# Kernel tuning notes

Measured on AMD Instinct MI355X. Metric: run time of the kernel, lower is better.

The kernel has to match this reference:

```python
import jax, jax.numpy as jnp
import numpy as np

B, M, N, D, H = 4, 8, 128, 32, 64
SMALL_V = 1e-8


def setup_inputs() -> dict:
    key = jax.random.key(0)
    ks = jax.random.split(key, 12)
    s = 0.05
    x = jax.random.normal(ks[0], (B, M, N, D), jnp.float32)
    sizes = jax.random.randint(ks[1], (B,), N // 2, N + 1)
    valid = (jnp.arange(N)[None, :] < sizes[:, None]).astype(jnp.float32)  # [B,N]
    x = x * valid[:, None, :, None]  # zero out padded items
    return {
        "x": x,
        "x_size": sizes.astype(jnp.float32),
        "W1a": jax.random.normal(ks[2], (D, 2 * D), jnp.float32) * s,
        "b1a": jax.random.normal(ks[3], (2 * D,), jnp.float32) * s,
        "W1b": jax.random.normal(ks[4], (2 * D, D), jnp.float32) * s,
        "b1b": jax.random.normal(ks[5], (D,), jnp.float32) * s,
        "W2a": jax.random.normal(ks[6], (D, 2 * D), jnp.float32) * s,
        "b2a": jax.random.normal(ks[7], (2 * D,), jnp.float32) * s,
        "W2b": jax.random.normal(ks[8], (2 * D, H), jnp.float32) * s,
        "b2b": jax.random.normal(ks[9], (H,), jnp.float32) * s,
        "w3": jax.random.normal(ks[10], (H,), jnp.float32) * s,
        "b3": jax.random.normal(ks[11], (1,), jnp.float32) * s,
    }


def _item_mask(x):
    # 1.0 where the item's feature row has any nonzero entry, else 0.0. [...,N,1]
    return jnp.any(x != 0, axis=-1, keepdims=True).astype(x.dtype)


def _set_norm(x, x_size):
    # layer_normalization with is_set_norm=True: normalize over (N*D) per set,
    # dividing by the true valid size x_size*D and masking padded items.
    b, m, n, d = x.shape
    mask = jnp.broadcast_to(_item_mask(x), x.shape).reshape(b, m, n * d)
    xr = x.reshape(b, m, n * d)
    denom = x_size[:, None] * d  # [B,1] -> broadcasts over nSet
    mean = jnp.sum(xr, axis=-1) / denom  # [B,M]
    diff = xr - mean[..., None]
    std = jnp.sqrt(jnp.sum(diff * diff * mask, axis=-1) / denom)  # [B,M]
    out = diff / (std[..., None] + SMALL_V) * mask
    return out.reshape(b, m, n, d)


def reference(x, x_size, W1a, b1a, W1b, b1b, W2a, b2a, W2b, b2b, w3, b3):
    mask = _item_mask(x)  # [B,M,N,1]
    x_orig = x
    xn = _set_norm(x, x_size) * mask  # [B,M,N,D]
    # MLP1 (rank-4 -> masked by its own input's item mask)
    m1 = _item_mask(xn)
    x1 = (jnp.matmul(jax.nn.gelu(jnp.matmul(xn, W1a) + b1a), W1b) + b1b) * m1
    # pairwise differences: x_diff[b,m,i,j,:] = x1[b,m,i,:] - xn[b,m,j,:]
    x_diff = x1[:, :, :, None, :] - xn[:, :, None, :, :]  # [B,M,N,N,D]
    # MLP2 (rank-5 -> no mask, is_SoftMax=0)
    e = jnp.matmul(jax.nn.gelu(jnp.matmul(x_diff, W2a) + b2a), W2b) + b2b  # [B,M,N,N,H]
    # aggregation: out[b,m,j,h,d] = sum_i e[b,m,i,j,h] * x1[b,m,i,d]
    agg = jnp.einsum('bmijh,bmid->bmjhd', e, x1)
    # MLP3_linear: Dense(1) over H, then squeeze
    out = jnp.einsum('bmjhd,h->bmjd', agg, w3) + b3[0]
    out = (out + x_orig) * mask
    return out
```

## Files before the change

kernel.cpp:

```cpp
#include <hip/hip_runtime.h>

#define NNC 128
#define DDC 32
#define KKC 64
constexpr int ND = NNC * DDC;
#define SMALLV 1e-8f

__device__ __forceinline__ float gelu_f(float v) {
    float v2 = v * v;
    float p  = fmaf(0.1029432f, v2, 2.3022082f);
    float e  = __builtin_amdgcn_exp2f(v * p);
    float r  = __builtin_amdgcn_rcpf(e + 1.0f);
    return fmaf(-v, r, v);
}

__global__ __launch_bounds__(512, 1) void fused3(
    const float* __restrict__ x, const float* __restrict__ x_size,
    const float* __restrict__ W1a, const float* __restrict__ b1a,
    const float* __restrict__ W1b, const float* __restrict__ b1b,
    const float* __restrict__ W2a, const float* __restrict__ b2a,
    const float* __restrict__ W2b, const float* __restrict__ b2b,
    const float* __restrict__ w3, const float* __restrict__ b3,
    float* __restrict__ out)
{
    __shared__ __align__(16) float smem[16384];

    const int t   = threadIdx.x;
    const int blk = blockIdx.x;
    const int bm  = blk >> 3;
    const int jt  = blk & 7;
    const int k   = t & 63;
    const int w   = t >> 6;
    const int dL  = t & 31;

    const int iN = (int)(x_size[bm >> 3] + 0.5f);

    float* sX1  = smem;
    float* sA1  = smem + 4096;
    float* sXn  = smem + 4096;
    float* sH32 = smem + 8192;
    float* scr  = smem + 12800;
    float* sA2t = smem + 12800;
    float* sSt  = smem + 13888;
    float* sV2  = smem + 16000;
    float* sAny = smem + 16064;
    float* sRed = smem + 16192;
    float* sC3  = smem + 16200;

    if (jt * 16 >= iN) {
        out[(size_t)bm * ND + jt * 512 + t] = 0.f;
        return;
    }

    float colA[32];
    #pragma unroll
    for (int d = 0; d < 32; ++d) colA[d] = W1a[d * 64 + k];
    float colB[64];
    #pragma unroll
    for (int q = 0; q < 64; ++q) colB[q] = W1b[q * 32 + dL];
    const float rb1a = b1a[k];
    const float rb1b = b1b[dL];
    const float rb2a = b2a[k];

    {
        const int kk = t >> 3, hq = t & 7;
        float p = 0.f;
        #pragma unroll
        for (int h = 0; h < 8; ++h)
            p = fmaf(W2b[kk * 64 + hq * 8 + h], w3[hq * 8 + h], p);
        scr[t] = p;
    }
    if (t < 64) {
        float q = b2b[t] * w3[t];
        #pragma unroll
        for (int off = 32; off; off >>= 1) q += __shfl_xor(q, off);
        if (t == 0) sC3[0] = q;
    }
    if (t < 128) sAny[t] = 0.f;
    __syncthreads();

    const float4* xs4 = (const float4*)(x + (size_t)bm * ND);
    float4 v4[2];
    float lsum = 0.f;
    #pragma unroll
    for (int s = 0; s < 2; ++s) {
        int f = t + s * 512;
        float4 q = xs4[f];
        v4[s] = q;
        lsum += q.x + q.y + q.z + q.w;
        if (q.x != 0.f || q.y != 0.f || q.z != 0.f || q.w != 0.f) sAny[f >> 3] = 1.f;
    }
    #pragma unroll
    for (int off = 32; off; off >>= 1) lsum += __shfl_xor(lsum, off);
    if ((t & 63) == 0) sRed[w] = lsum;
    __syncthreads();
    if (t < 64) {
        float vp = 0.f;
        #pragma unroll
        for (int q = 0; q < 8; ++q) vp += scr[t * 8 + q];
        sV2[t] = vp;
    }
    const float denom = x_size[bm >> 3] * 32.f;
    float mean = 0.f;
    #pragma unroll
    for (int r = 0; r < 8; ++r) mean += sRed[r];
    mean /= denom;

    float lsq = 0.f;
    #pragma unroll
    for (int s = 0; s < 2; ++s) {
        int f = t + s * 512;
        float mk = sAny[f >> 3];
        float dx = v4[s].x - mean, dy = v4[s].y - mean;
        float dz = v4[s].z - mean, dw = v4[s].w - mean;
        lsq += mk * (dx * dx + dy * dy + dz * dz + dw * dw);
    }
    #pragma unroll
    for (int off = 32; off; off >>= 1) lsq += __shfl_xor(lsq, off);
    __syncthreads();
    if ((t & 63) == 0) sRed[w] = lsq;
    __syncthreads();
    float sq = 0.f;
    #pragma unroll
    for (int r = 0; r < 8; ++r) sq += sRed[r];
    const float inv = 1.f / (sqrtf(sq / denom) + SMALLV);

    #pragma unroll
    for (int s = 0; s < 2; ++s) {
        int f = t + s * 512;
        float mk = sAny[f >> 3] * inv;
        float4 q = v4[s];
        q.x = (q.x - mean) * mk; q.y = (q.y - mean) * mk;
        q.z = (q.z - mean) * mk; q.w = (q.w - mean) * mk;
        ((float4*)sXn)[f] = q;
    }
    __syncthreads();

    for (int c = 0; c < 4; ++c) {
        const int rb = c * 32;
        const bool live = (rb < iN);
        if (live) {
            #pragma unroll
            for (int r = 0; r < 4; ++r) {
                const int nl = w + 8 * r;
                const float4* xr4 = (const float4*)&sXn[(rb + nl) * 32];
                float acc = rb1a;
                #pragma unroll
                for (int dq = 0; dq < 8; ++dq) {
                    float4 xv = xr4[dq];
                    acc = fmaf(xv.x, colA[4 * dq + 0], acc);
                    acc = fmaf(xv.y, colA[4 * dq + 1], acc);
                    acc = fmaf(xv.z, colA[4 * dq + 2], acc);
                    acc = fmaf(xv.w, colA[4 * dq + 3], acc);
                }
                sH32[nl * 64 + k] = gelu_f(acc);
            }
        }
        __syncthreads();
        if (live) {
            #pragma unroll
            for (int p = 0; p < 2; ++p) {
                const int nl = (t >> 5) + 16 * p;
                const float4* hr4 = (const float4*)&sH32[nl * 64];
                float acc = rb1b;
                #pragma unroll
                for (int qq = 0; qq < 16; ++qq) {
                    float4 hv = hr4[qq];
                    acc = fmaf(hv.x, colB[4 * qq + 0], acc);
                    acc = fmaf(hv.y, colB[4 * qq + 1], acc);
                    acc = fmaf(hv.z, colB[4 * qq + 2], acc);
                    acc = fmaf(hv.w, colB[4 * qq + 3], acc);
                }
                sX1[(rb + nl) * 32 + dL] = acc * sAny[rb + nl];
            }
        } else {
            #pragma unroll
            for (int p = 0; p < 2; ++p)
                sX1[(rb + (t >> 5) + 16 * p) * 32 + dL] = 0.f;
        }
        __syncthreads();
    }

    float colC[32];
    #pragma unroll
    for (int d = 0; d < 32; ++d) colC[d] = W2a[d * 64 + k];
    #pragma unroll
    for (int q = 0; q < 2; ++q) {
        const int jl = w + 8 * q;
        const float4* xr4 = (const float4*)&sXn[(jt * 16 + jl) * 32];
        float acc = 0.f;
        #pragma unroll
        for (int dq = 0; dq < 8; ++dq) {
            float4 xv = xr4[dq];
            acc = fmaf(xv.x, colC[4 * dq + 0], acc);
            acc = fmaf(xv.y, colC[4 * dq + 1], acc);
            acc = fmaf(xv.z, colC[4 * dq + 2], acc);
            acc = fmaf(xv.w, colC[4 * dq + 3], acc);
        }
        sA2t[jl * 68 + k] = acc;
    }
    __syncthreads();

    const int ICAP = (iN + 3) & ~3;
    for (int n = w; n < ICAP; n += 8) {
        const float4* x14 = (const float4*)&sX1[n * 32];
        float acc = rb2a;
        #pragma unroll
        for (int dq = 0; dq < 8; ++dq) {
            float4 xv = x14[dq];
            acc = fmaf(xv.x, colC[4 * dq + 0], acc);
            acc = fmaf(xv.y, colC[4 * dq + 1], acc);
            acc = fmaf(xv.z, colC[4 * dq + 2], acc);
            acc = fmaf(xv.w, colC[4 * dq + 3], acc);
        }
        sA1[n * 68 + k] = acc;
    }
    __syncthreads();

    {
        const float c3 = sC3[0];
        const int j  = t & 15;
        const int i0 = (t >> 4) * 4;
        if (i0 < iN) {
            float a0 = c3, a1 = c3, a2 = c3, a3 = c3;
            const float* a2row = &sA2t[j * 68];
            const float* b0r = &sA1[(i0 + 0) * 68];
            const float* b1r = &sA1[(i0 + 1) * 68];
            const float* b2r = &sA1[(i0 + 2) * 68];
            const float* b3r = &sA1[(i0 + 3) * 68];
            #pragma unroll 4
            for (int kk = 0; kk < 64; kk += 4) {
                float4 va = *(const float4*)&a2row[kk];
                float4 vv = *(const float4*)&sV2[kk];
                float4 q0 = *(const float4*)&b0r[kk];
                float4 q1 = *(const float4*)&b1r[kk];
                float4 q2 = *(const float4*)&b2r[kk];
                float4 q3 = *(const float4*)&b3r[kk];
                a0 = fmaf(gelu_f(q0.x - va.x), vv.x, a0);
                a1 = fmaf(gelu_f(q1.x - va.x), vv.x, a1);
                a2 = fmaf(gelu_f(q2.x - va.x), vv.x, a2);
                a3 = fmaf(gelu_f(q3.x - va.x), vv.x, a3);
                a0 = fmaf(gelu_f(q0.y - va.y), vv.y, a0);
                a1 = fmaf(gelu_f(q1.y - va.y), vv.y, a1);
                a2 = fmaf(gelu_f(q2.y - va.y), vv.y, a2);
                a3 = fmaf(gelu_f(q3.y - va.y), vv.y, a3);
                a0 = fmaf(gelu_f(q0.z - va.z), vv.z, a0);
                a1 = fmaf(gelu_f(q1.z - va.z), vv.z, a1);
                a2 = fmaf(gelu_f(q2.z - va.z), vv.z, a2);
                a3 = fmaf(gelu_f(q3.z - va.z), vv.z, a3);
                a0 = fmaf(gelu_f(q0.w - va.w), vv.w, a0);
                a1 = fmaf(gelu_f(q1.w - va.w), vv.w, a1);
                a2 = fmaf(gelu_f(q2.w - va.w), vv.w, a2);
                a3 = fmaf(gelu_f(q3.w - va.w), vv.w, a3);
            }
            *(float4*)&sSt[j * 132 + i0] = make_float4(a0, a1, a2, a3);
        }
    }
    __syncthreads();

    {
        const int jA = t >> 5;
        const int dA = t & 31;
        const float* strow = &sSt[jA * 132];
        float s0 = 0.f;
        for (int i = 0; i < ICAP; i += 4) {
            float4 sv = *(const float4*)&strow[i];
            s0 = fmaf(sv.x, sX1[(i + 0) * 32 + dA], s0);
            s0 = fmaf(sv.y, sX1[(i + 1) * 32 + dA], s0);
            s0 = fmaf(sv.z, sX1[(i + 2) * 32 + dA], s0);
            s0 = fmaf(sv.w, sX1[(i + 3) * 32 + dA], s0);
        }
        const int jg = jt * 16 + jA;
        const float msk = sAny[jg];
        const size_t ob = (size_t)bm * ND + jg * 32 + dA;
        out[ob] = (s0 + b3[0] + x[ob]) * msk;
    }
}

extern "C" void kernel_launch(void* const* d_in, const int* in_sizes, int n_in,
                              void* d_out, int out_size, void* d_ws, size_t ws_size,
                              hipStream_t stream) {
    (void)in_sizes; (void)n_in; (void)d_ws; (void)ws_size; (void)out_size;
    const float* x      = (const float*)d_in[0];
    const float* x_size = (const float*)d_in[1];
    const float* W1a    = (const float*)d_in[2];
    const float* b1a    = (const float*)d_in[3];
    const float* W1b    = (const float*)d_in[4];
    const float* b1b    = (const float*)d_in[5];
    const float* W2a    = (const float*)d_in[6];
    const float* b2a    = (const float*)d_in[7];
    const float* W2b    = (const float*)d_in[8];
    const float* b2b    = (const float*)d_in[9];
    const float* w3     = (const float*)d_in[10];
    const float* b3     = (const float*)d_in[11];
    float* out = (float*)d_out;

    fused3<<<dim3(256), dim3(512), 0, stream>>>(
        x, x_size, W1a, b1a, W1b, b1b, W2a, b2a, W2b, b2b, w3, b3, out);
}
```

Measured before the change: 99.42 us.

## Double block size to 1024 threads and rescope weight registers per phase

```diff
diff --git a/kernel.cpp b/kernel.cpp
--- a/kernel.cpp
+++ b/kernel.cpp
@@ -14,7 +14,7 @@
     return fmaf(-v, r, v);
 }
 
-__global__ __launch_bounds__(512, 1) void fused3(
+__global__ __launch_bounds__(1024, 4) void fused4(
     const float* __restrict__ x, const float* __restrict__ x_size,
     const float* __restrict__ W1a, const float* __restrict__ b1a,
     const float* __restrict__ W1b, const float* __restrict__ b1b,
@@ -38,36 +38,30 @@
     float* sX1  = smem;
     float* sA1  = smem + 4096;
     float* sXn  = smem + 4096;
-    float* sH32 = smem + 8192;
-    float* scr  = smem + 12800;
+    float* sH64 = smem + 8192;
     float* sA2t = smem + 12800;
     float* sSt  = smem + 13888;
+    float* scr  = smem + 13888;
     float* sV2  = smem + 16000;
     float* sAny = smem + 16064;
     float* sRed = smem + 16192;
-    float* sC3  = smem + 16200;
+    float* sC3  = smem + 16208;
 
     if (jt * 16 >= iN) {
-        out[(size_t)bm * ND + jt * 512 + t] = 0.f;
+        if (t < 512) out[(size_t)bm * ND + jt * 512 + t] = 0.f;
         return;
     }
 
-    float colA[32];
-    #pragma unroll
-    for (int d = 0; d < 32; ++d) colA[d] = W1a[d * 64 + k];
-    float colB[64];
-    #pragma unroll
-    for (int q = 0; q < 64; ++q) colB[q] = W1b[q * 32 + dL];
     const float rb1a = b1a[k];
     const float rb1b = b1b[dL];
     const float rb2a = b2a[k];
 
     {
-        const int kk = t >> 3, hq = t & 7;
+        const int kk = t >> 4, hq = t & 15;
         float p = 0.f;
         #pragma unroll
-        for (int h = 0; h < 8; ++h)
-            p = fmaf(W2b[kk * 64 + hq * 8 + h], w3[hq * 8 + h], p);
+        for (int h = 0; h < 4; ++h)
+            p = fmaf(W2b[kk * 64 + hq * 4 + h], w3[hq * 4 + h], p);
         scr[t] = p;
     }
     if (t < 64) {
@@ -80,16 +74,10 @@
     __syncthreads();
 
     const float4* xs4 = (const float4*)(x + (size_t)bm * ND);
-    float4 v4[2];
-    float lsum = 0.f;
-    #pragma unroll
-    for (int s = 0; s < 2; ++s) {
-        int f = t + s * 512;
-        float4 q = xs4[f];
-        v4[s] = q;
-        lsum += q.x + q.y + q.z + q.w;
-        if (q.x != 0.f || q.y != 0.f || q.z != 0.f || q.w != 0.f) sAny[f >> 3] = 1.f;
-    }
+    float4 xv4 = xs4[t];
+    float lsum = xv4.x + xv4.y + xv4.z + xv4.w;
+    if (xv4.x != 0.f || xv4.y != 0.f || xv4.z != 0.f || xv4.w != 0.f)
+        sAny[t >> 3] = 1.f;
     #pragma unroll
     for (int off = 32; off; off >>= 1) lsum += __shfl_xor(lsum, off);
     if ((t & 63) == 0) sRed[w] = lsum;
@@ -97,23 +85,21 @@
     if (t < 64) {
         float vp = 0.f;
         #pragma unroll
-        for (int q = 0; q < 8; ++q) vp += scr[t * 8 + q];
+        for (int q = 0; q < 16; ++q) vp += scr[t * 16 + q];
         sV2[t] = vp;
     }
     const float denom = x_size[bm >> 3] * 32.f;
     float mean = 0.f;
     #pragma unroll
-    for (int r = 0; r < 8; ++r) mean += sRed[r];
+    for (int r = 0; r < 16; ++r) mean += sRed[r];
     mean /= denom;
 
-    float lsq = 0.f;
-    #pragma unroll
-    for (int s = 0; s < 2; ++s) {
-        int f = t + s * 512;
-        float mk = sAny[f >> 3];
-        float dx = v4[s].x - mean, dy = v4[s].y - mean;
-        float dz = v4[s].z - mean, dw = v4[s].w - mean;
-        lsq += mk * (dx * dx + dy * dy + dz * dz + dw * dw);
+    float lsq;
+    {
+        const float mk = sAny[t >> 3];
+        const float dx = xv4.x - mean, dy = xv4.y - mean;
+        const float dz = xv4.z - mean, dw = xv4.w - mean;
+        lsq = mk * (dx * dx + dy * dy + dz * dz + dw * dw);
     }
     #pragma unroll
     for (int off = 32; off; off >>= 1) lsq += __shfl_xor(lsq, off);
@@ -122,61 +108,69 @@
     __syncthreads();
     float sq = 0.f;
     #pragma unroll
-    for (int r = 0; r < 8; ++r) sq += sRed[r];
+    for (int r = 0; r < 16; ++r) sq += sRed[r];
     const float inv = 1.f / (sqrtf(sq / denom) + SMALLV);
 
-    #pragma unroll
-    for (int s = 0; s < 2; ++s) {
-        int f = t + s * 512;
-        float mk = sAny[f >> 3] * inv;
-        float4 q = v4[s];
+    {
+        const float mk = sAny[t >> 3] * inv;
+        float4 q = xv4;
         q.x = (q.x - mean) * mk; q.y = (q.y - mean) * mk;
         q.z = (q.z - mean) * mk; q.w = (q.w - mean) * mk;
-        ((float4*)sXn)[f] = q;
-    }
-    __syncthreads();
-
-    for (int c = 0; c < 4; ++c) {
-        const int rb = c * 32;
+        ((float4*)sXn)[t] = q;
+    }
+    __syncthreads();
+
+    for (int c = 0; c < 2; ++c) {
+        const int rb = c * 64;
         const bool live = (rb < iN);
-        if (live) {
+        {
+            float colA[32];
             #pragma unroll
-            for (int r = 0; r < 4; ++r) {
-                const int nl = w + 8 * r;
-                const float4* xr4 = (const float4*)&sXn[(rb + nl) * 32];
-                float acc = rb1a;
+            for (int d = 0; d < 32; ++d) colA[d] = W1a[d * 64 + k];
+            if (live) {
                 #pragma unroll
-                for (int dq = 0; dq < 8; ++dq) {
-                    float4 xv = xr4[dq];
-                    acc = fmaf(xv.x, colA[4 * dq + 0], acc);
-                    acc = fmaf(xv.y, colA[4 * dq + 1], acc);
-                    acc = fmaf(xv.z, colA[4 * dq + 2], acc);
-                    acc = fmaf(xv.w, colA[4 * dq + 3], acc);
+                for (int r = 0; r < 4; ++r) {
+                    const int nl = w + 16 * r;
+                    const float4* xr4 = (const float4*)&sXn[(rb + nl) * 32];
+                    float acc = rb1a;
+                    #pragma unroll
+                    for (int dq = 0; dq < 8; ++dq) {
+                        float4 xv = xr4[dq];
+                        acc = fmaf(xv.x, colA[4 * dq + 0], acc);
+                        acc = fmaf(xv.y, colA[4 * dq + 1], acc);
+                        acc = fmaf(xv.z, colA[4 * dq + 2], acc);
+                        acc = fmaf(xv.w, colA[4 * dq + 3], acc);
+                    }
+                    sH64[nl * 64 + k] = gelu_f(acc);
                 }
-                sH32[nl * 64 + k] = gelu_f(acc);
             }
         }
         __syncthreads();
-        if (live) {
+        {
+            float colB[64];
             #pragma unroll
-            for (int p = 0; p < 2; ++p) {
-                const int nl = (t >> 5) + 16 * p;
-                const float4* hr4 = (const float4*)&sH32[nl * 64];
-                float acc = rb1b;
+            for (int q2 = 0; q2 < 64; ++q2) colB[q2] = W1b[q2 * 32 + dL];
+            if (live) {
                 #pragma unroll
-                for (int qq = 0; qq < 16; ++qq) {
-                    float4 hv = hr4[qq];
-                    acc = fmaf(hv.x, colB[4 * qq + 0], acc);
-                    acc = fmaf(hv.y, colB[4 * qq + 1], acc);
-                    acc = fmaf(hv.z, colB[4 * qq + 2], acc);
-                    acc = fmaf(hv.w, colB[4 * qq + 3], acc);
+                for (int p = 0; p < 2; ++p) {
+                    const int nl = (t >> 5) + 32 * p;
+                    const float4* hr4 = (const float4*)&sH64[nl * 64];
+                    float acc = rb1b;
+                    #pragma unroll
+                    for (int qq = 0; qq < 16; ++qq) {
+                        float4 hv = hr4[qq];
+                        acc = fmaf(hv.x, colB[4 * qq + 0], acc);
+                        acc = fmaf(hv.y, colB[4 * qq + 1], acc);
+                        acc = fmaf(hv.z, colB[4 * qq + 2], acc);
+                        acc = fmaf(hv.w, colB[4 * qq + 3], acc);
+                    }
+                    sX1[(rb + nl) * 32 + dL] = acc * sAny[rb + nl];
                 }
-                sX1[(rb + nl) * 32 + dL] = acc * sAny[rb + nl];
+            } else {
+                #pragma unroll
+                for (int p = 0; p < 2; ++p)
+                    sX1[(rb + (t >> 5) + 32 * p) * 32 + dL] = 0.f;
             }
-        } else {
-            #pragma unroll
-            for (int p = 0; p < 2; ++p)
-                sX1[(rb + (t >> 5) + 16 * p) * 32 + dL] = 0.f;
         }
         __syncthreads();
     }
@@ -184,10 +178,8 @@
     float colC[32];
     #pragma unroll
     for (int d = 0; d < 32; ++d) colC[d] = W2a[d * 64 + k];
-    #pragma unroll
-    for (int q = 0; q < 2; ++q) {
-        const int jl = w + 8 * q;
-        const float4* xr4 = (const float4*)&sXn[(jt * 16 + jl) * 32];
+    {
+        const float4* xr4 = (const float4*)&sXn[(jt * 16 + w) * 32];
         float acc = 0.f;
         #pragma unroll
         for (int dq = 0; dq < 8; ++dq) {
@@ -197,12 +189,12 @@
             acc = fmaf(xv.z, colC[4 * dq + 2], acc);
             acc = fmaf(xv.w, colC[4 * dq + 3], acc);
         }
-        sA2t[jl * 68 + k] = acc;
+        sA2t[w * 68 + k] = acc;
     }
     __syncthreads();
 
     const int ICAP = (iN + 3) & ~3;
-    for (int n = w; n < ICAP; n += 8) {
+    for (int n = w; n < ICAP; n += 16) {
         const float4* x14 = (const float4*)&sX1[n * 32];
         float acc = rb2a;
         #pragma unroll
@@ -220,45 +212,33 @@
     {
         const float c3 = sC3[0];
         const int j  = t & 15;
-        const int i0 = (t >> 4) * 4;
-        if (i0 < iN) {
-            float a0 = c3, a1 = c3, a2 = c3, a3 = c3;
+        const int i0 = (t >> 4) * 2;
+        if (i0 < ICAP) {
+            float a0 = c3, a1 = c3;
             const float* a2row = &sA2t[j * 68];
             const float* b0r = &sA1[(i0 + 0) * 68];
             const float* b1r = &sA1[(i0 + 1) * 68];
-            const float* b2r = &sA1[(i0 + 2) * 68];
-            const float* b3r = &sA1[(i0 + 3) * 68];
             #pragma unroll 4
             for (int kk = 0; kk < 64; kk += 4) {
                 float4 va = *(const float4*)&a2row[kk];
                 float4 vv = *(const float4*)&sV2[kk];
                 float4 q0 = *(const float4*)&b0r[kk];
                 float4 q1 = *(const float4*)&b1r[kk];
-                float4 q2 = *(const float4*)&b2r[kk];
-                float4 q3 = *(const float4*)&b3r[kk];
                 a0 = fmaf(gelu_f(q0.x - va.x), vv.x, a0);
                 a1 = fmaf(gelu_f(q1.x - va.x), vv.x, a1);
-                a2 = fmaf(gelu_f(q2.x - va.x), vv.x, a2);
-                a3 = fmaf(gelu_f(q3.x - va.x), vv.x, a3);
                 a0 = fmaf(gelu_f(q0.y - va.y), vv.y, a0);
                 a1 = fmaf(gelu_f(q1.y - va.y), vv.y, a1);
-                a2 = fmaf(gelu_f(q2.y - va.y), vv.y, a2);
-                a3 = fmaf(gelu_f(q3.y - va.y), vv.y, a3);
                 a0 = fmaf(gelu_f(q0.z - va.z), vv.z, a0);
                 a1 = fmaf(gelu_f(q1.z - va.z), vv.z, a1);
-                a2 = fmaf(gelu_f(q2.z - va.z), vv.z, a2);
-                a3 = fmaf(gelu_f(q3.z - va.z), vv.z, a3);
                 a0 = fmaf(gelu_f(q0.w - va.w), vv.w, a0);
                 a1 = fmaf(gelu_f(q1.w - va.w), vv.w, a1);
-                a2 = fmaf(gelu_f(q2.w - va.w), vv.w, a2);
-                a3 = fmaf(gelu_f(q3.w - va.w), vv.w, a3);
             }
-            *(float4*)&sSt[j * 132 + i0] = make_float4(a0, a1, a2, a3);
-        }
-    }
-    __syncthreads();
-
-    {
+            *(float2*)&sSt[j * 132 + i0] = make_float2(a0, a1);
+        }
+    }
+    __syncthreads();
+
+    if (t < 512) {
         const int jA = t >> 5;
         const int dA = t & 31;
         const float* strow = &sSt[jA * 132];
@@ -295,6 +275,6 @@
     const float* b3     = (const float*)d_in[11];
     float* out = (float*)d_out;
 
-    fused3<<<dim3(256), dim3(512), 0, stream>>>(
+    fused4<<<dim3(256), dim3(1024), 0, stream>>>(
         x, x_size, W1a, b1a, W1b, b1b, W2a, b2a, W2b, b2b, w3, b3, out);
 }
```

New measurement: 100.6 us. About the same (+1.2%).
